# Kernel optimization log

Hardware: AMD Instinct MI355X
Metric: run time of the kernel (lower is better)

## Reference

```python
import jax, jax.numpy as jnp
import numpy as np

B, T, N_IN, N = 64, 512, 256, 512

def setup_inputs() -> dict:
    key = jax.random.key(0)
    k1, k2, k3 = jax.random.split(key, 3)
    x = jax.random.normal(k1, (B, T, N_IN), dtype=jnp.float32)
    # match nn.Linear default init scale roughly (uniform +-1/sqrt(fan_in))
    W_ih = jax.random.uniform(k2, (N, N_IN), dtype=jnp.float32, minval=-1.0, maxval=1.0) / np.sqrt(N_IN)
    W_hh = jax.random.uniform(k3, (N, N), dtype=jnp.float32, minval=-1.0, maxval=1.0) / np.sqrt(N)
    return {"x": x, "W_ih": W_ih, "W_hh": W_hh}

def reference(x, W_ih, W_hh):
    # h_t = W_hh @ tanh(h_{t-1}) + W_ih @ x_t, h_0 = 0 (pre-activation hidden stored)
    # x: [B, T, n_in] (batch_first). Precompute input projections for all steps.
    xp = jnp.einsum('btc,nc->tbn', x, W_ih)  # [T, B, N]

    def step(h, xp_t):
        h_new = jnp.tanh(h) @ W_hh.T + xp_t  # [B, N]
        return h_new, h_new

    h0 = jnp.zeros((x.shape[0], W_hh.shape[0]), dtype=x.dtype)
    _, hs = jax.lax.scan(step, h0, xp)  # hs: [T, B, N]
    return jnp.swapaxes(hs, 0, 1)  # [B, T, N], batch_first output
```

## Files before the change

### kernel.cpp

```cpp
#include <hip/hip_runtime.h>
#include <hip/hip_bf16.h>
#include <stdint.h>

#define B_   64
#define T_   512
#define NIN_ 256
#define N_   512

typedef _Float16 half2_t __attribute__((ext_vector_type(2)));

#if defined(__has_builtin)
#if __has_builtin(__builtin_amdgcn_fdot2)
#define HAVE_FDOT2 1
#endif
#endif

__device__ __forceinline__ float dot2acc(unsigned int a, unsigned int b, float c) {
#ifdef HAVE_FDOT2
  return __builtin_amdgcn_fdot2(__builtin_bit_cast(half2_t, a),
                                __builtin_bit_cast(half2_t, b), c, false);
#else
  half2_t ha = __builtin_bit_cast(half2_t, a), hb = __builtin_bit_cast(half2_t, b);
  c += (float)ha[0] * (float)hb[0];
  c += (float)ha[1] * (float)hb[1];
  return c;
#endif
}

__device__ __forceinline__ float fast_tanh(float x) {
  float e = __expf(2.0f * x);
  return 1.0f - 2.0f / (e + 1.0f);
}

__device__ __forceinline__ unsigned int packh2(float a, float b) {
  half2_t h;
  h[0] = (_Float16)a;
  h[1] = (_Float16)b;
  return __builtin_bit_cast(unsigned int, h);
}

__device__ __forceinline__ int thp_idx(int p) {
  return (((p >> 2) & 15) << 4) + ((p >> 6) << 2) + (p & 3);
}

__global__ __launch_bounds__(256) void xproj(const float* __restrict__ x,
                                             const float* __restrict__ Wih,
                                             float* __restrict__ out) {
  const int tid = threadIdx.x;
  const int bm = blockIdx.x;
  const int bn = blockIdx.y;
  const int tm = tid & 15;
  const int tn = tid >> 4;
  const int m0 = bm << 7;
  const int n0 = bn << 7;

  __shared__ float xt[32][132];
  __shared__ float wt[32][132];

  float acc[8][8];
#pragma unroll
  for (int i = 0; i < 8; ++i)
#pragma unroll
    for (int j = 0; j < 8; ++j) acc[i][j] = 0.f;

  for (int ko = 0; ko < NIN_; ko += 32) {
#pragma unroll
    for (int it = 0; it < 4; ++it) {
      const int fidx = it * 256 + tid;
      const int mm = fidx >> 3;
      const int k4 = (fidx & 7) << 2;
      const float4 vx = *(const float4*)(x + (size_t)(m0 + mm) * NIN_ + ko + k4);
      xt[k4 + 0][mm] = vx.x; xt[k4 + 1][mm] = vx.y;
      xt[k4 + 2][mm] = vx.z; xt[k4 + 3][mm] = vx.w;
      const float4 vw = *(const float4*)(Wih + (size_t)(n0 + mm) * NIN_ + ko + k4);
      wt[k4 + 0][mm] = vw.x; wt[k4 + 1][mm] = vw.y;
      wt[k4 + 2][mm] = vw.z; wt[k4 + 3][mm] = vw.w;
    }
    __syncthreads();
#pragma unroll 4
    for (int kk = 0; kk < 32; ++kk) {
      float a[8], b[8];
      *(float4*)&a[0] = *(const float4*)&xt[kk][8 * tm];
      *(float4*)&a[4] = *(const float4*)&xt[kk][8 * tm + 4];
      *(float4*)&b[0] = *(const float4*)&wt[kk][8 * tn];
      *(float4*)&b[4] = *(const float4*)&wt[kk][8 * tn + 4];
#pragma unroll
      for (int i = 0; i < 8; ++i)
#pragma unroll
        for (int j = 0; j < 8; ++j) acc[i][j] = fmaf(a[i], b[j], acc[i][j]);
    }
    __syncthreads();
  }

#pragma unroll
  for (int i = 0; i < 8; ++i) {
    float4 v0 = make_float4(acc[i][0], acc[i][1], acc[i][2], acc[i][3]);
    float4 v1 = make_float4(acc[i][4], acc[i][5], acc[i][6], acc[i][7]);
    float* p = out + (size_t)(m0 + 8 * tm + i) * N_ + n0 + 8 * tn;
    *(float4*)p = v0;
    *((float4*)p + 1) = v1;
  }
}

__global__ __launch_bounds__(512) void rnn_scan(const float* __restrict__ Whh,
                                                float* __restrict__ out,
                                                unsigned long long* __restrict__ ex) {
  const int blk = blockIdx.x;
  const int xcd = blk & 7;
  const int rest = blk >> 3;
  const int m = rest & 3;
  const int b = xcd + ((rest >> 2) << 3);
  const int tid = threadIdx.x;
  const int wv = tid >> 6;
  const int lane = tid & 63;
  const int q = lane & 3;
  const int nn = wv * 16 + (lane >> 2);
  const int gn = m * 128 + nn;

  __shared__ __align__(16) unsigned int thp[2][256];

  float* outb = out + (size_t)b * T_ * N_;
  unsigned long long* exb = ex + (size_t)b * 1024;

  unsigned int w[64];
  {
    const float* wr = Whh + (size_t)gn * N_ + q * 128;
#pragma unroll
    for (int j = 0; j < 64; ++j) {
      float2 v = *(const float2*)(wr + 2 * j);
      w[j] = packh2(v.x, v.y);
    }
  }

  if (tid < 256) {
    float2 h0 = *(const float2*)(outb + 2 * tid);
    thp[0][thp_idx(tid)] = packh2(fast_tanh(h0.x), fast_tanh(h0.y));
  }

  const int pv = tid & 127;
  const int sr = tid >> 7;
  const int sm = sr + (sr >= m ? 1 : 0);
  const int prn = sm * 128 + pv;

  __syncthreads();

  for (int t = 1; t < T_; ++t) {
    float xp = 0.f;
    if (q == 0) xp = outb[(size_t)t * N_ + gn];

    if (t >= 2 && tid < 384) {
      unsigned long long v;
      do {
        v = __hip_atomic_load(&exb[((t - 1) & 1) * 512 + prn],
                              __ATOMIC_RELAXED, __HIP_MEMORY_SCOPE_AGENT);
      } while ((unsigned int)(v >> 32) != (unsigned int)(t - 1));
      const float th = fast_tanh(__uint_as_float((unsigned int)v));
      const float thn = __shfl_xor(th, 1);
      if ((tid & 1) == 0) thp[(t - 1) & 1][thp_idx(prn >> 1)] = packh2(th, thn);
    }
    __syncthreads();

    const uint4* tq = (const uint4*)&thp[(t - 1) & 1][0];
    float acc = 0.f;
#pragma unroll
    for (int j4 = 0; j4 < 16; ++j4) {
      const uint4 tv = tq[j4 * 4 + q];
      acc = dot2acc(w[4 * j4 + 0], tv.x, acc);
      acc = dot2acc(w[4 * j4 + 1], tv.y, acc);
      acc = dot2acc(w[4 * j4 + 2], tv.z, acc);
      acc = dot2acc(w[4 * j4 + 3], tv.w, acc);
    }
    acc += __shfl_xor(acc, 1);
    acc += __shfl_xor(acc, 2);

    float th_own = 0.f;
    if (q == 0) {
      const float y = acc + xp;
      __hip_atomic_store(&exb[(t & 1) * 512 + gn],
                         ((unsigned long long)(unsigned int)t << 32) |
                             (unsigned long long)__float_as_uint(y),
                         __ATOMIC_RELAXED, __HIP_MEMORY_SCOPE_AGENT);
      __builtin_nontemporal_store(y, &outb[(size_t)t * N_ + gn]);
      th_own = fast_tanh(y);
    }
    const float th_nb = __shfl_xor(th_own, 4);
    if ((lane & 7) == 0)
      thp[t & 1][thp_idx(gn >> 1)] = packh2(th_own, th_nb);
  }
}

extern "C" void kernel_launch(void* const* d_in, const int* in_sizes, int n_in,
                              void* d_out, int out_size, void* d_ws, size_t ws_size,
                              hipStream_t stream) {
  const float* x   = (const float*)d_in[0];
  const float* Wih = (const float*)d_in[1];
  const float* Whh = (const float*)d_in[2];
  float* out = (float*)d_out;
  unsigned long long* ex = (unsigned long long*)d_ws;

  hipMemsetAsync(d_ws, 0, (size_t)B_ * 2 * 512 * 8, stream);

  dim3 g1(256, 4);
  xproj<<<g1, 256, 0, stream>>>(x, Wih, out);
  rnn_scan<<<256, 512, 0, stream>>>(Whh, out, ex);
}
```

Measured before the change: 760.2 us.

## Fuse input projection and recurrence into one kernel using MFMA and time-chunked flags

Merges the input-projection GEMM and the recurrent scan into a single persistent launch. 128 blocks compute the projection in time chunks and publish per-chunk completion counters, and the other 128 blocks start the recurrence as soon as their chunk is ready. The recurrence moves from per-lane fdot2 dot products to 16x16x32 f16 MFMA, with each block handling 4 batch rows and 64 neurons. Tanh is now applied before exchange, so peers send packed fp16 activations instead of raw floats. This is meant to overlap the GEMM with the scan and to cut per-step latency. The risks are the extra cross-block synchronisation, the reliance on all 256 blocks being co-resident, and a reduction step through LDS.

```diff
diff --git a/kernel.cpp b/kernel.cpp
--- a/kernel.cpp
+++ b/kernel.cpp
@@ -1,5 +1,4 @@
 #include <hip/hip_runtime.h>
-#include <hip/hip_bf16.h>
 #include <stdint.h>
 
 #define B_   64
@@ -7,185 +6,202 @@
 #define NIN_ 256
 #define N_   512
 
+typedef _Float16 half8   __attribute__((ext_vector_type(8)));
+typedef float    f32x4   __attribute__((ext_vector_type(4)));
 typedef _Float16 half2_t __attribute__((ext_vector_type(2)));
-
-#if defined(__has_builtin)
-#if __has_builtin(__builtin_amdgcn_fdot2)
-#define HAVE_FDOT2 1
-#endif
-#endif
-
-__device__ __forceinline__ float dot2acc(unsigned int a, unsigned int b, float c) {
-#ifdef HAVE_FDOT2
-  return __builtin_amdgcn_fdot2(__builtin_bit_cast(half2_t, a),
-                                __builtin_bit_cast(half2_t, b), c, false);
-#else
-  half2_t ha = __builtin_bit_cast(half2_t, a), hb = __builtin_bit_cast(half2_t, b);
-  c += (float)ha[0] * (float)hb[0];
-  c += (float)ha[1] * (float)hb[1];
-  return c;
-#endif
-}
 
 __device__ __forceinline__ float fast_tanh(float x) {
   float e = __expf(2.0f * x);
   return 1.0f - 2.0f / (e + 1.0f);
 }
-
 __device__ __forceinline__ unsigned int packh2(float a, float b) {
-  half2_t h;
-  h[0] = (_Float16)a;
-  h[1] = (_Float16)b;
+  half2_t h; h[0] = (_Float16)a; h[1] = (_Float16)b;
   return __builtin_bit_cast(unsigned int, h);
 }
 
-__device__ __forceinline__ int thp_idx(int p) {
-  return (((p >> 2) & 15) << 4) + ((p >> 6) << 2) + (p & 3);
-}
-
-__global__ __launch_bounds__(256) void xproj(const float* __restrict__ x,
-                                             const float* __restrict__ Wih,
-                                             float* __restrict__ out) {
+__global__ __launch_bounds__(1024, 4) void rnn_fused(
+    const float* __restrict__ x, const float* __restrict__ Wih,
+    const float* __restrict__ Whh, float* __restrict__ out,
+    unsigned long long* __restrict__ ex, int* __restrict__ ctrl) {
+  const int blk = blockIdx.x;
   const int tid = threadIdx.x;
-  const int bm = blockIdx.x;
-  const int bn = blockIdx.y;
-  const int tm = tid & 15;
-  const int tn = tid >> 4;
-  const int m0 = bm << 7;
-  const int n0 = bn << 7;
 
   __shared__ float xt[32][132];
   __shared__ float wt[32][132];
-
-  float acc[8][8];
-#pragma unroll
-  for (int i = 0; i < 8; ++i)
-#pragma unroll
-    for (int j = 0; j < 8; ++j) acc[i][j] = 0.f;
-
-  for (int ko = 0; ko < NIN_; ko += 32) {
-#pragma unroll
-    for (int it = 0; it < 4; ++it) {
-      const int fidx = it * 256 + tid;
-      const int mm = fidx >> 3;
-      const int k4 = (fidx & 7) << 2;
-      const float4 vx = *(const float4*)(x + (size_t)(m0 + mm) * NIN_ + ko + k4);
-      xt[k4 + 0][mm] = vx.x; xt[k4 + 1][mm] = vx.y;
-      xt[k4 + 2][mm] = vx.z; xt[k4 + 3][mm] = vx.w;
-      const float4 vw = *(const float4*)(Wih + (size_t)(n0 + mm) * NIN_ + ko + k4);
-      wt[k4 + 0][mm] = vw.x; wt[k4 + 1][mm] = vw.y;
-      wt[k4 + 2][mm] = vw.z; wt[k4 + 3][mm] = vw.w;
-    }
-    __syncthreads();
+  __shared__ __align__(16) unsigned int th_lds[2][4][260];
+  __shared__ __align__(16) float pacc[4][4][16][4];
+
+  if (blk < 128) {
+    const int tm = tid & 15;
+    const int tn = tid >> 4;
+    for (int tau = blk; tau < 1024; tau += 128) {
+      const int tc = tau >> 8;
+      const int j  = tau & 255;
+      const int bb = j >> 2;
+      const int bn = j & 3;
+      const int m0 = (bb * 4 + tc) << 7;
+      const int nn0 = bn << 7;
+
+      float acc[8][2];
+#pragma unroll
+      for (int i = 0; i < 8; ++i) { acc[i][0] = 0.f; acc[i][1] = 0.f; }
+
+      for (int ko = 0; ko < NIN_; ko += 32) {
+        const int mm = tid >> 3;
+        const int k4 = (tid & 7) << 2;
+        const float4 vx = *(const float4*)(x + (size_t)(m0 + mm) * NIN_ + ko + k4);
+        xt[k4 + 0][mm] = vx.x; xt[k4 + 1][mm] = vx.y;
+        xt[k4 + 2][mm] = vx.z; xt[k4 + 3][mm] = vx.w;
+        const float4 vw = *(const float4*)(Wih + (size_t)(nn0 + mm) * NIN_ + ko + k4);
+        wt[k4 + 0][mm] = vw.x; wt[k4 + 1][mm] = vw.y;
+        wt[k4 + 2][mm] = vw.z; wt[k4 + 3][mm] = vw.w;
+        __syncthreads();
 #pragma unroll 4
-    for (int kk = 0; kk < 32; ++kk) {
-      float a[8], b[8];
-      *(float4*)&a[0] = *(const float4*)&xt[kk][8 * tm];
-      *(float4*)&a[4] = *(const float4*)&xt[kk][8 * tm + 4];
-      *(float4*)&b[0] = *(const float4*)&wt[kk][8 * tn];
-      *(float4*)&b[4] = *(const float4*)&wt[kk][8 * tn + 4];
-#pragma unroll
-      for (int i = 0; i < 8; ++i)
-#pragma unroll
-        for (int j = 0; j < 8; ++j) acc[i][j] = fmaf(a[i], b[j], acc[i][j]);
-    }
-    __syncthreads();
-  }
-
-#pragma unroll
-  for (int i = 0; i < 8; ++i) {
-    float4 v0 = make_float4(acc[i][0], acc[i][1], acc[i][2], acc[i][3]);
-    float4 v1 = make_float4(acc[i][4], acc[i][5], acc[i][6], acc[i][7]);
-    float* p = out + (size_t)(m0 + 8 * tm + i) * N_ + n0 + 8 * tn;
-    *(float4*)p = v0;
-    *((float4*)p + 1) = v1;
-  }
-}
-
-__global__ __launch_bounds__(512) void rnn_scan(const float* __restrict__ Whh,
-                                                float* __restrict__ out,
-                                                unsigned long long* __restrict__ ex) {
-  const int blk = blockIdx.x;
-  const int xcd = blk & 7;
-  const int rest = blk >> 3;
-  const int m = rest & 3;
-  const int b = xcd + ((rest >> 2) << 3);
-  const int tid = threadIdx.x;
+        for (int kk = 0; kk < 32; ++kk) {
+          float a[8];
+          *(float4*)&a[0] = *(const float4*)&xt[kk][8 * tm];
+          *(float4*)&a[4] = *(const float4*)&xt[kk][8 * tm + 4];
+          const float2 bv = *(const float2*)&wt[kk][2 * tn];
+#pragma unroll
+          for (int i = 0; i < 8; ++i) {
+            acc[i][0] = fmaf(a[i], bv.x, acc[i][0]);
+            acc[i][1] = fmaf(a[i], bv.y, acc[i][1]);
+          }
+        }
+        __syncthreads();
+      }
+#pragma unroll
+      for (int i = 0; i < 8; ++i) {
+        float2 st; st.x = acc[i][0]; st.y = acc[i][1];
+        *(float2*)(out + (size_t)(m0 + 8 * tm + i) * N_ + nn0 + 2 * tn) = st;
+      }
+      __threadfence();
+      __syncthreads();
+      if (tid == 0)
+        __hip_atomic_fetch_add(&ctrl[tc], 1, __ATOMIC_RELEASE,
+                               __HIP_MEMORY_SCOPE_AGENT);
+    }
+    return;
+  }
+
+  const int beta = blk - 128;
+  const int g = beta & 15;
+  const int m = beta >> 4;
+  const int gB = g * 4;
+  const int ns = m * 64;
+
   const int wv = tid >> 6;
-  const int lane = tid & 63;
-  const int q = lane & 3;
-  const int nn = wv * 16 + (lane >> 2);
-  const int gn = m * 128 + nn;
-
-  __shared__ __align__(16) unsigned int thp[2][256];
-
-  float* outb = out + (size_t)b * T_ * N_;
-  unsigned long long* exb = ex + (size_t)b * 1024;
-
-  unsigned int w[64];
+  const int l  = tid & 63;
+  const int nr = wv >> 2;
+  const int kq = wv & 3;
+  const int c  = l & 15;
+  const int o  = l >> 4;
+
+  const int arow = ns + nr * 16 + c;
+  const float* wb = Whh + (size_t)arow * N_ + kq * 128 + o * 8;
+#define LDW(TAU)                                                       \
+  half8 wf##TAU;                                                       \
+  {                                                                    \
+    const float* wr = wb + (TAU) * 32;                                 \
+    const float4 w0 = *(const float4*)wr;                              \
+    const float4 w1 = *(const float4*)(wr + 4);                        \
+    wf##TAU[0] = (_Float16)w0.x; wf##TAU[1] = (_Float16)w0.y;          \
+    wf##TAU[2] = (_Float16)w0.z; wf##TAU[3] = (_Float16)w0.w;          \
+    wf##TAU[4] = (_Float16)w1.x; wf##TAU[5] = (_Float16)w1.y;          \
+    wf##TAU[6] = (_Float16)w1.z; wf##TAU[7] = (_Float16)w1.w;          \
+  }
+  LDW(0) LDW(1) LDW(2) LDW(3)
+#undef LDW
+  asm volatile("" : "+v"(wf0), "+v"(wf1), "+v"(wf2), "+v"(wf3));
+
+  const int enr = tid >> 6;
+  const int eb  = (tid >> 4) & 3;
+  const int erow = tid & 15;
+  const size_t outrow_e = (size_t)(gB + eb) * T_ * N_;
+  const int eneuron = ns + enr * 16 + erow;
+  const int rm = tid >> 7;
+  const int rr = tid & 127;
+  const int pb = rr >> 5;
+  const int pp = rr & 31;
+  const int sm = rm + (rm >= m ? 1 : 0);
+
+  if (tid == 0) {
+    while (__hip_atomic_load(&ctrl[0], __ATOMIC_ACQUIRE,
+                             __HIP_MEMORY_SCOPE_AGENT) < 256)
+      __builtin_amdgcn_s_sleep(1);
+  }
+  __syncthreads();
   {
-    const float* wr = Whh + (size_t)gn * N_ + q * 128;
-#pragma unroll
-    for (int j = 0; j < 64; ++j) {
-      float2 v = *(const float2*)(wr + 2 * j);
-      w[j] = packh2(v.x, v.y);
-    }
-  }
-
-  if (tid < 256) {
-    float2 h0 = *(const float2*)(outb + 2 * tid);
-    thp[0][thp_idx(tid)] = packh2(fast_tanh(h0.x), fast_tanh(h0.y));
-  }
-
-  const int pv = tid & 127;
-  const int sr = tid >> 7;
-  const int sm = sr + (sr >= m ? 1 : 0);
-  const int prn = sm * 128 + pv;
-
+    const int b0 = tid >> 8;
+    const int c0 = tid & 255;
+    const float2 h0 = *(const float2*)(out + (size_t)(gB + b0) * T_ * N_ + 2 * c0);
+    th_lds[0][b0][c0] = packh2(fast_tanh(h0.x), fast_tanh(h0.y));
+  }
   __syncthreads();
 
   for (int t = 1; t < T_; ++t) {
+    if ((t & 127) == 0) {
+      if (tid == 0) {
+        while (__hip_atomic_load(&ctrl[t >> 7], __ATOMIC_ACQUIRE,
+                                 __HIP_MEMORY_SCOPE_AGENT) < 256)
+          __builtin_amdgcn_s_sleep(1);
+      }
+      __syncthreads();
+    }
+
     float xp = 0.f;
-    if (q == 0) xp = outb[(size_t)t * N_ + gn];
-
-    if (t >= 2 && tid < 384) {
+    if (tid < 256) xp = out[outrow_e + (size_t)t * N_ + eneuron];
+
+    if (t >= 2 && tid < 896) {
+      const unsigned long long* ap =
+          &ex[((((size_t)g * 2 + ((t - 1) & 1)) * 8 + sm) * 4 + pb) * 32 + pp];
       unsigned long long v;
       do {
-        v = __hip_atomic_load(&exb[((t - 1) & 1) * 512 + prn],
-                              __ATOMIC_RELAXED, __HIP_MEMORY_SCOPE_AGENT);
+        v = __hip_atomic_load(ap, __ATOMIC_RELAXED, __HIP_MEMORY_SCOPE_AGENT);
       } while ((unsigned int)(v >> 32) != (unsigned int)(t - 1));
-      const float th = fast_tanh(__uint_as_float((unsigned int)v));
-      const float thn = __shfl_xor(th, 1);
-      if ((tid & 1) == 0) thp[(t - 1) & 1][thp_idx(prn >> 1)] = packh2(th, thn);
+      th_lds[(t - 1) & 1][pb][sm * 32 + pp] = (unsigned int)v;
     }
     __syncthreads();
 
-    const uint4* tq = (const uint4*)&thp[(t - 1) & 1][0];
-    float acc = 0.f;
-#pragma unroll
-    for (int j4 = 0; j4 < 16; ++j4) {
-      const uint4 tv = tq[j4 * 4 + q];
-      acc = dot2acc(w[4 * j4 + 0], tv.x, acc);
-      acc = dot2acc(w[4 * j4 + 1], tv.y, acc);
-      acc = dot2acc(w[4 * j4 + 2], tv.z, acc);
-      acc = dot2acc(w[4 * j4 + 3], tv.w, acc);
-    }
-    acc += __shfl_xor(acc, 1);
-    acc += __shfl_xor(acc, 2);
+    {
+      const unsigned int* tb = &th_lds[(t - 1) & 1][c & 3][kq * 64 + o * 4];
+      f32x4 acc = {0.f, 0.f, 0.f, 0.f};
+#define MM(TAU)                                                            \
+  {                                                                        \
+    const uint4 bv = *(const uint4*)(tb + (TAU) * 16);                     \
+    acc = __builtin_amdgcn_mfma_f32_16x16x32_f16(                          \
+        wf##TAU, __builtin_bit_cast(half8, bv), acc, 0, 0, 0);             \
+  }
+      MM(0) MM(1) MM(2) MM(3)
+#undef MM
+      if (c < 4) {
+#pragma unroll
+        for (int jj = 0; jj < 4; ++jj)
+          pacc[nr][c][(o << 2) + jj][kq] = acc[jj];
+      }
+    }
+    __syncthreads();
 
     float th_own = 0.f;
-    if (q == 0) {
-      const float y = acc + xp;
-      __hip_atomic_store(&exb[(t & 1) * 512 + gn],
-                         ((unsigned long long)(unsigned int)t << 32) |
-                             (unsigned long long)__float_as_uint(y),
-                         __ATOMIC_RELAXED, __HIP_MEMORY_SCOPE_AGENT);
-      __builtin_nontemporal_store(y, &outb[(size_t)t * N_ + gn]);
+    float y = 0.f;
+    if (tid < 256) {
+      const float4 pv = *(const float4*)&pacc[enr][eb][erow][0];
+      y = pv.x + pv.y + pv.z + pv.w + xp;
       th_own = fast_tanh(y);
     }
-    const float th_nb = __shfl_xor(th_own, 4);
-    if ((lane & 7) == 0)
-      thp[t & 1][thp_idx(gn >> 1)] = packh2(th_own, th_nb);
+    const float th_nb = __shfl_xor(th_own, 1);
+    if (tid < 256) {
+      if ((erow & 1) == 0) {
+        const unsigned int pk = packh2(th_own, th_nb);
+        const int po = (enr * 16 + erow) >> 1;
+        __hip_atomic_store(
+            &ex[((((size_t)g * 2 + (t & 1)) * 8 + m) * 4 + eb) * 32 + po],
+            ((unsigned long long)(unsigned int)t << 32) | pk,
+            __ATOMIC_RELAXED, __HIP_MEMORY_SCOPE_AGENT);
+        th_lds[t & 1][eb][m * 32 + po] = pk;
+      }
+      __builtin_nontemporal_store(y, &out[outrow_e + (size_t)t * N_ + eneuron]);
+    }
   }
 }
 
@@ -197,10 +213,8 @@
   const float* Whh = (const float*)d_in[2];
   float* out = (float*)d_out;
   unsigned long long* ex = (unsigned long long*)d_ws;
-
-  hipMemsetAsync(d_ws, 0, (size_t)B_ * 2 * 512 * 8, stream);
-
-  dim3 g1(256, 4);
-  xproj<<<g1, 256, 0, stream>>>(x, Wih, out);
-  rnn_scan<<<256, 512, 0, stream>>>(Whh, out, ex);
-}
+  int* ctrl = (int*)((char*)d_ws + 262144);
+
+  hipMemsetAsync(d_ws, 0, 262144 + 64, stream);
+  rnn_fused<<<256, 1024, 0, stream>>>(x, Wih, Whh, out, ex, ctrl);
+}
```

Result: slower. 1.574 ms (+107.0%).
